# Kernel optimization log

Measured on AMD Instinct MI355X. Metric: run time of the kernel, lower is better.

## Reference

```python
import jax, jax.numpy as jnp
import numpy as np

N_NODES = 50000
N_EDGES = 600000
N_GRAPHS = 500
HID = 128
N_LAYERS = 3
N_CLASSES = 10


def setup_inputs() -> dict:
    key = jax.random.key(0)
    ks = jax.random.split(key, 10)
    x = jax.random.normal(ks[0], (N_NODES, HID), dtype=jnp.float32)
    edge_attr = jax.random.normal(ks[1], (N_EDGES, 4), dtype=jnp.float32)
    edge_index = jax.random.randint(ks[2], (2, N_EDGES), 0, N_NODES, dtype=jnp.int32)
    batch = jnp.sort(jax.random.randint(ks[3], (N_NODES,), 0, N_GRAPHS, dtype=jnp.int32))
    s = 1.0 / np.sqrt(HID)
    Wl = jax.random.normal(ks[4], (N_LAYERS, HID, HID), dtype=jnp.float32) * s
    bl = jax.random.normal(ks[5], (N_LAYERS, HID), dtype=jnp.float32) * s
    Wr = jax.random.normal(ks[6], (N_LAYERS, HID, HID), dtype=jnp.float32) * s
    W1 = jax.random.normal(ks[7], (HID, HID), dtype=jnp.float32) * s
    b1 = jnp.zeros((HID,), dtype=jnp.float32)
    W2 = jax.random.normal(ks[8], (N_CLASSES, HID), dtype=jnp.float32) * s
    b2 = jnp.zeros((N_CLASSES,), dtype=jnp.float32)
    return {"x": x, "edge_attr": edge_attr, "edge_index": edge_index, "batch": batch,
            "Wl": Wl, "bl": bl, "Wr": Wr, "W1": W1, "b1": b1, "W2": W2, "b2": b2}


def _sage_conv(x, src, dst, Wl_i, bl_i, Wr_i):
    # mean aggregation of source-node features at target nodes (PyG SAGEConv)
    msg_sum = jax.ops.segment_sum(x[src], dst, num_segments=N_NODES)  # [N, H]
    cnt = jax.ops.segment_sum(jnp.ones((src.shape[0],), x.dtype), dst, num_segments=N_NODES)
    mean = msg_sum / jnp.maximum(cnt, 1.0)[:, None]
    return mean @ Wl_i.T + bl_i + x @ Wr_i.T


def reference(x, edge_attr, edge_index, batch, Wl, bl, Wr, W1, b1, W2, b2):
    # edge_attr is ignored by SAGEConv
    src, dst = edge_index[0], edge_index[1]
    for i in range(N_LAYERS):
        x = jax.nn.relu(_sage_conv(x, src, dst, Wl[i], bl[i], Wr[i]))
    # global_add_pool over graphs
    g = jax.ops.segment_sum(x, batch, num_segments=N_GRAPHS)  # [G, H]
    g = jax.nn.relu(g)
    # dropout p=0.5 is identity at inference
    h = jax.nn.relu(g @ W1.T + b1)
    logits = h @ W2.T + b2
    return jax.nn.log_softmax(logits, axis=1)
```

## Files before the change

kernel.cpp:

```cpp
#include <hip/hip_runtime.h>
#include <math.h>

#define HID 128
#define NCLS 10
#define MAXDEG 32

typedef __attribute__((ext_vector_type(8))) short frag8;
typedef __attribute__((ext_vector_type(8))) unsigned short u16x8;
typedef __attribute__((ext_vector_type(4))) float f32x4;

static __device__ __forceinline__ float relu_f(float v) { return v > 0.f ? v : 0.f; }

static __device__ __forceinline__ unsigned short f2bf(float f) {
    unsigned int u = __float_as_uint(f);
    u += 0x7fffu + ((u >> 16) & 1u);
    return (unsigned short)(u >> 16);
}
static __device__ __forceinline__ float bf2f(unsigned short u) {
    return __uint_as_float(((unsigned int)u) << 16);
}

static __device__ __forceinline__ void conv4(const float* __restrict__ in,
                                             unsigned short* __restrict__ out, int i) {
    float4 v = *(const float4*)&in[i * 4];
    ushort4 o;
    o.x = f2bf(v.x); o.y = f2bf(v.y); o.z = f2bf(v.z); o.w = f2bf(v.w);
    *(ushort4*)&out[i * 4] = o;
}

__global__ __launch_bounds__(256) void prep_kernel(const float* __restrict__ x, unsigned short* __restrict__ xb, int nx4,
                                                   const float* __restrict__ Wl, unsigned short* __restrict__ wlb, int nwl4,
                                                   const float* __restrict__ Wr, unsigned short* __restrict__ wrb, int nwr4,
                                                   int* __restrict__ deg, int ndeg4) {
    int i = blockIdx.x * blockDim.x + threadIdx.x;
    if (i < nx4) { conv4(x, xb, i); return; }
    i -= nx4;
    if (i < nwl4) { conv4(Wl, wlb, i); return; }
    i -= nwl4;
    if (i < nwr4) { conv4(Wr, wrb, i); return; }
    i -= nwr4;
    if (i < ndeg4) *(int4*)&deg[i * 4] = make_int4(0, 0, 0, 0);
}

__global__ void fill_kernel(const int* __restrict__ src, const int* __restrict__ dst,
                            int* __restrict__ deg, unsigned short* __restrict__ col, int nE) {
    int e = blockIdx.x * blockDim.x + threadIdx.x;
    if (e < nE) {
        int d = dst[e];
        int p = atomicAdd(&deg[d], 1);
        if (p < MAXDEG) col[(long)d * MAXDEG + p] = (unsigned short)src[e];
    }
}

__global__ __launch_bounds__(256) void agg_kernel(const unsigned short* __restrict__ xb,
                                                  const int* __restrict__ deg,
                                                  const unsigned short* __restrict__ col,
                                                  unsigned short* __restrict__ meanb, int nN) {
    int grp = threadIdx.x >> 4;
    int l16 = threadIdx.x & 15;
    int n = blockIdx.x * 16 + grp;
    bool valid = n < nN;
    int d = valid ? min(deg[n], MAXDEG) : 0;
    const unsigned short* cp = col + (long)n * MAXDEG;
    const long fo = (long)l16 * 8;

    float acc[8] = {0, 0, 0, 0, 0, 0, 0, 0};

    int p = 0;
    for (; p + 8 <= d; p += 8) {
        int s0 = cp[p],     s1 = cp[p + 1], s2 = cp[p + 2], s3 = cp[p + 3];
        int s4 = cp[p + 4], s5 = cp[p + 5], s6 = cp[p + 6], s7 = cp[p + 7];
        u16x8 v0 = *(const u16x8*)&xb[(long)s0 * HID + fo];
        u16x8 v1 = *(const u16x8*)&xb[(long)s1 * HID + fo];
        u16x8 v2 = *(const u16x8*)&xb[(long)s2 * HID + fo];
        u16x8 v3 = *(const u16x8*)&xb[(long)s3 * HID + fo];
        u16x8 v4 = *(const u16x8*)&xb[(long)s4 * HID + fo];
        u16x8 v5 = *(const u16x8*)&xb[(long)s5 * HID + fo];
        u16x8 v6 = *(const u16x8*)&xb[(long)s6 * HID + fo];
        u16x8 v7 = *(const u16x8*)&xb[(long)s7 * HID + fo];
#pragma unroll
        for (int j = 0; j < 8; ++j)
            acc[j] += ((bf2f(v0[j]) + bf2f(v1[j])) + (bf2f(v2[j]) + bf2f(v3[j]))) +
                      ((bf2f(v4[j]) + bf2f(v5[j])) + (bf2f(v6[j]) + bf2f(v7[j])));
    }
    if (p + 4 <= d) {
        int s0 = cp[p], s1 = cp[p + 1], s2 = cp[p + 2], s3 = cp[p + 3];
        u16x8 v0 = *(const u16x8*)&xb[(long)s0 * HID + fo];
        u16x8 v1 = *(const u16x8*)&xb[(long)s1 * HID + fo];
        u16x8 v2 = *(const u16x8*)&xb[(long)s2 * HID + fo];
        u16x8 v3 = *(const u16x8*)&xb[(long)s3 * HID + fo];
#pragma unroll
        for (int j = 0; j < 8; ++j)
            acc[j] += (bf2f(v0[j]) + bf2f(v1[j])) + (bf2f(v2[j]) + bf2f(v3[j]));
        p += 4;
    }
    if (p < d) {
        int s0 = cp[p];
        int s1 = cp[min(p + 1, MAXDEG - 1)];
        int s2 = cp[min(p + 2, MAXDEG - 1)];
        int s3 = cp[min(p + 3, MAXDEG - 1)];
        u16x8 v0 = *(const u16x8*)&xb[(long)s0 * HID + fo];
        u16x8 v1 = *(const u16x8*)&xb[(long)s1 * HID + fo];
        u16x8 v2 = *(const u16x8*)&xb[(long)s2 * HID + fo];
        u16x8 v3 = *(const u16x8*)&xb[(long)s3 * HID + fo];
#pragma unroll
        for (int j = 0; j < 8; ++j) acc[j] += bf2f(v0[j]);
        if (p + 1 < d) {
#pragma unroll
            for (int j = 0; j < 8; ++j) acc[j] += bf2f(v1[j]);
        }
        if (p + 2 < d) {
#pragma unroll
            for (int j = 0; j < 8; ++j) acc[j] += bf2f(v2[j]);
        }
        if (p + 3 < d) {
#pragma unroll
            for (int j = 0; j < 8; ++j) acc[j] += bf2f(v3[j]);
        }
    }

    if (valid) {
        float inv = 1.f / fmaxf((float)d, 1.f);
        u16x8 o;
#pragma unroll
        for (int j = 0; j < 8; ++j) o[j] = f2bf(acc[j] * inv);
        *(u16x8*)&meanb[(long)n * HID + fo] = o;
    }
}

__global__ __launch_bounds__(256) void gemm_kernel(const unsigned short* __restrict__ Ab,
                                                   const unsigned short* __restrict__ Xb,
                                                   const unsigned short* __restrict__ Wlb,
                                                   const unsigned short* __restrict__ Wrb,
                                                   const float* __restrict__ bl,
                                                   unsigned short* __restrict__ Yb, int nN) {
    int wave = threadIdx.x >> 6;
    int lane = threadIdx.x & 63;
    int l15 = lane & 15;
    int quad = lane >> 4;
    int r0 = blockIdx.x * 128 + wave * 32;

    f32x4 acc[2][8];
#pragma unroll
    for (int rt = 0; rt < 2; ++rt)
#pragma unroll
        for (int ct = 0; ct < 8; ++ct) acc[rt][ct] = (f32x4){0.f, 0.f, 0.f, 0.f};

#pragma unroll
    for (int ks = 0; ks < HID; ks += 32) {
        frag8 aM[2], aX[2];
#pragma unroll
        for (int rt = 0; rt < 2; ++rt) {
            long row = r0 + rt * 16 + l15;
            aM[rt] = *(const frag8*)&Ab[row * HID + ks + quad * 8];
            aX[rt] = *(const frag8*)&Xb[row * HID + ks + quad * 8];
        }
#pragma unroll
        for (int ct = 0; ct < 8; ++ct) {
            long nrow = ct * 16 + l15;
            frag8 bL = *(const frag8*)&Wlb[nrow * HID + ks + quad * 8];
            frag8 bR = *(const frag8*)&Wrb[nrow * HID + ks + quad * 8];
#pragma unroll
            for (int rt = 0; rt < 2; ++rt) {
                acc[rt][ct] = __builtin_amdgcn_mfma_f32_16x16x32_bf16(aM[rt], bL, acc[rt][ct], 0, 0, 0);
                acc[rt][ct] = __builtin_amdgcn_mfma_f32_16x16x32_bf16(aX[rt], bR, acc[rt][ct], 0, 0, 0);
            }
        }
    }

#pragma unroll
    for (int ct = 0; ct < 8; ++ct) {
        float bb = bl[ct * 16 + l15];
#pragma unroll
        for (int rt = 0; rt < 2; ++rt) {
#pragma unroll
            for (int reg = 0; reg < 4; ++reg) {
                int gm = r0 + rt * 16 + quad * 4 + reg;
                if (gm < nN) {
                    float v = relu_f(acc[rt][ct][reg] + bb);
                    Yb[(long)gm * HID + ct * 16 + l15] = f2bf(v);
                }
            }
        }
    }
}

__global__ __launch_bounds__(128) void poolmlp_kernel(const unsigned short* __restrict__ xb,
                                                      const int* __restrict__ batch, int nN,
                                                      const float* __restrict__ W1,
                                                      const float* __restrict__ b1,
                                                      const float* __restrict__ W2,
                                                      const float* __restrict__ b2,
                                                      float* __restrict__ out) {
    __shared__ float gs[HID];
    __shared__ float hs[HID];
    __shared__ float ls[NCLS];
    __shared__ float red[2];
    int gid = blockIdx.x;
    int j = threadIdx.x;

    int lo = 0, hi = nN;
    while (lo < hi) { int mid = (lo + hi) >> 1; if (batch[mid] < gid) lo = mid + 1; else hi = mid; }
    int s = lo;
    hi = nN;
    while (lo < hi) { int mid = (lo + hi) >> 1; if (batch[mid] < gid + 1) lo = mid + 1; else hi = mid; }
    int e = lo;

    float a0 = 0.f, a1 = 0.f, a2 = 0.f, a3 = 0.f;
    int n = s;
    for (; n + 4 <= e; n += 4) {
        a0 += bf2f(xb[(long)n * HID + j]);
        a1 += bf2f(xb[(long)(n + 1) * HID + j]);
        a2 += bf2f(xb[(long)(n + 2) * HID + j]);
        a3 += bf2f(xb[(long)(n + 3) * HID + j]);
    }
    for (; n < e; ++n) a0 += bf2f(xb[(long)n * HID + j]);
    gs[j] = relu_f((a0 + a1) + (a2 + a3));
    __syncthreads();

    float acc = b1[j];
#pragma unroll 8
    for (int k = 0; k < HID; ++k) acc += gs[k] * W1[j * HID + k];
    hs[j] = relu_f(acc);
    __syncthreads();
    if (j < NCLS) {
        float lg = b2[j];
#pragma unroll 8
        for (int k = 0; k < HID; ++k) lg += hs[k] * W2[j * HID + k];
        ls[j] = lg;
    }
    __syncthreads();
    if (j == 0) {
        float m = ls[0];
        for (int c = 1; c < NCLS; ++c) m = fmaxf(m, ls[c]);
        float sum = 0.f;
        for (int c = 0; c < NCLS; ++c) sum += expf(ls[c] - m);
        red[0] = m;
        red[1] = logf(sum);
    }
    __syncthreads();
    if (j < NCLS) out[gid * NCLS + j] = ls[j] - red[0] - red[1];
}


extern "C" void kernel_launch(void* const* d_in, const int* in_sizes, int n_in,
                              void* d_out, int out_size, void* d_ws, size_t ws_size,
                              hipStream_t stream) {
    const float* x_in  = (const float*)d_in[0];
    const int*   eidx  = (const int*)d_in[2];
    const int*   batch = (const int*)d_in[3];
    const float* Wl    = (const float*)d_in[4];
    const float* bl    = (const float*)d_in[5];
    const float* Wr    = (const float*)d_in[6];
    const float* W1    = (const float*)d_in[7];
    const float* b1    = (const float*)d_in[8];
    const float* W2    = (const float*)d_in[9];
    const float* b2    = (const float*)d_in[10];
    float* out = (float*)d_out;

    const int nN = in_sizes[0] / HID;
    const int nE = in_sizes[2] / 2;
    const int nG = out_size / NCLS;
    const int nWl = in_sizes[4];
    const int nWr = in_sizes[6];
    const int nNp = (nN + 127) & ~127;
    const int nTiles = nNp / 128;

    const int* src = eidx;
    const int* dst = eidx + nE;

    char* p = (char*)d_ws;
    auto carve = [&](size_t bytes) {
        char* r = p;
        p += (bytes + 255) & ~(size_t)255;
        return r;
    };
    unsigned short* xb    = (unsigned short*)carve((size_t)nNp * HID * 2);
    unsigned short* meanb = (unsigned short*)carve((size_t)nNp * HID * 2);
    unsigned short* yb0   = (unsigned short*)carve((size_t)nNp * HID * 2);
    unsigned short* yb1   = (unsigned short*)carve((size_t)nNp * HID * 2);
    unsigned short* wlb   = (unsigned short*)carve((size_t)nWl * 2);
    unsigned short* wrb   = (unsigned short*)carve((size_t)nWr * 2);
    int*   deg    = (int*)carve((size_t)nN * 4);
    unsigned short* col = (unsigned short*)carve((size_t)nN * MAXDEG * 2);
    (void)ws_size; (void)n_in;

    const int nx4 = nN * HID / 4, nwl4 = nWl / 4, nwr4 = nWr / 4, ndeg4 = (nN + 3) / 4;
    const int prep_total = nx4 + nwl4 + nwr4 + ndeg4;
    prep_kernel<<<(prep_total + 255) / 256, 256, 0, stream>>>(
        x_in, xb, nx4, Wl, wlb, nwl4, Wr, wrb, nwr4, deg, ndeg4);

    fill_kernel<<<(nE + 255) / 256, 256, 0, stream>>>(src, dst, deg, col, nE);

    const unsigned short* xcur = xb;
    unsigned short* bufs[2] = {yb0, yb1};
    for (int l = 0; l < 3; ++l) {
        agg_kernel<<<(nN + 15) / 16, 256, 0, stream>>>(xcur, deg, col, meanb, nN);
        gemm_kernel<<<nTiles, 256, 0, stream>>>(
            meanb, xcur, wlb + (size_t)l * HID * HID, wrb + (size_t)l * HID * HID,
            bl + (size_t)l * HID, bufs[l & 1], nN);
        xcur = bufs[l & 1];
    }

    poolmlp_kernel<<<nG, 128, 0, stream>>>(xcur, batch, nN, W1, b1, W2, b2, out);
}
```

Measured before the change: 307.6 us.

## Fuse neighbor mean aggregation into SAGE GEMM via shared-memory tile

Merges the separate aggregation and GEMM kernels into one kernel per layer. Each block gathers the mean features for 64 rows into padded shared memory, syncs, then runs the bf16 MFMA GEMM with four waves split 2x2 over rows and output columns. This drops the global round trip of the mean buffer and one launch per layer. In exchange, tiles are smaller, each block serializes gather latency before its MFMA phase, and the shared-memory tile may limit occupancy.

```diff
diff --git a/kernel.cpp b/kernel.cpp
--- a/kernel.cpp
+++ b/kernel.cpp
@@ -4,6 +4,8 @@
 #define HID 128
 #define NCLS 10
 #define MAXDEG 32
+#define TROWS 64
+#define MSP 136
 
 typedef __attribute__((ext_vector_type(8))) short frag8;
 typedef __attribute__((ext_vector_type(8))) unsigned short u16x8;
@@ -52,112 +54,116 @@
     }
 }
 
-__global__ __launch_bounds__(256) void agg_kernel(const unsigned short* __restrict__ xb,
-                                                  const int* __restrict__ deg,
-                                                  const unsigned short* __restrict__ col,
-                                                  unsigned short* __restrict__ meanb, int nN) {
-    int grp = threadIdx.x >> 4;
-    int l16 = threadIdx.x & 15;
-    int n = blockIdx.x * 16 + grp;
-    bool valid = n < nN;
-    int d = valid ? min(deg[n], MAXDEG) : 0;
-    const unsigned short* cp = col + (long)n * MAXDEG;
-    const long fo = (long)l16 * 8;
-
-    float acc[8] = {0, 0, 0, 0, 0, 0, 0, 0};
-
-    int p = 0;
-    for (; p + 8 <= d; p += 8) {
-        int s0 = cp[p],     s1 = cp[p + 1], s2 = cp[p + 2], s3 = cp[p + 3];
-        int s4 = cp[p + 4], s5 = cp[p + 5], s6 = cp[p + 6], s7 = cp[p + 7];
-        u16x8 v0 = *(const u16x8*)&xb[(long)s0 * HID + fo];
-        u16x8 v1 = *(const u16x8*)&xb[(long)s1 * HID + fo];
-        u16x8 v2 = *(const u16x8*)&xb[(long)s2 * HID + fo];
-        u16x8 v3 = *(const u16x8*)&xb[(long)s3 * HID + fo];
-        u16x8 v4 = *(const u16x8*)&xb[(long)s4 * HID + fo];
-        u16x8 v5 = *(const u16x8*)&xb[(long)s5 * HID + fo];
-        u16x8 v6 = *(const u16x8*)&xb[(long)s6 * HID + fo];
-        u16x8 v7 = *(const u16x8*)&xb[(long)s7 * HID + fo];
-#pragma unroll
-        for (int j = 0; j < 8; ++j)
-            acc[j] += ((bf2f(v0[j]) + bf2f(v1[j])) + (bf2f(v2[j]) + bf2f(v3[j]))) +
-                      ((bf2f(v4[j]) + bf2f(v5[j])) + (bf2f(v6[j]) + bf2f(v7[j])));
-    }
-    if (p + 4 <= d) {
-        int s0 = cp[p], s1 = cp[p + 1], s2 = cp[p + 2], s3 = cp[p + 3];
-        u16x8 v0 = *(const u16x8*)&xb[(long)s0 * HID + fo];
-        u16x8 v1 = *(const u16x8*)&xb[(long)s1 * HID + fo];
-        u16x8 v2 = *(const u16x8*)&xb[(long)s2 * HID + fo];
-        u16x8 v3 = *(const u16x8*)&xb[(long)s3 * HID + fo];
-#pragma unroll
-        for (int j = 0; j < 8; ++j)
-            acc[j] += (bf2f(v0[j]) + bf2f(v1[j])) + (bf2f(v2[j]) + bf2f(v3[j]));
-        p += 4;
-    }
-    if (p < d) {
-        int s0 = cp[p];
-        int s1 = cp[min(p + 1, MAXDEG - 1)];
-        int s2 = cp[min(p + 2, MAXDEG - 1)];
-        int s3 = cp[min(p + 3, MAXDEG - 1)];
-        u16x8 v0 = *(const u16x8*)&xb[(long)s0 * HID + fo];
-        u16x8 v1 = *(const u16x8*)&xb[(long)s1 * HID + fo];
-        u16x8 v2 = *(const u16x8*)&xb[(long)s2 * HID + fo];
-        u16x8 v3 = *(const u16x8*)&xb[(long)s3 * HID + fo];
-#pragma unroll
-        for (int j = 0; j < 8; ++j) acc[j] += bf2f(v0[j]);
-        if (p + 1 < d) {
-#pragma unroll
-            for (int j = 0; j < 8; ++j) acc[j] += bf2f(v1[j]);
+__global__ __launch_bounds__(256, 3) void sage_kernel(const unsigned short* __restrict__ Xb,
+                                                      const int* __restrict__ deg,
+                                                      const unsigned short* __restrict__ col,
+                                                      const unsigned short* __restrict__ Wlb,
+                                                      const unsigned short* __restrict__ Wrb,
+                                                      const float* __restrict__ bl,
+                                                      unsigned short* __restrict__ Yb, int nN) {
+    __shared__ unsigned short ms[TROWS * MSP];
+
+    const int r0 = blockIdx.x * TROWS;
+
+    {
+        const int grp = threadIdx.x >> 4;
+        const int l16 = threadIdx.x & 15;
+        const long fo = (long)l16 * 8;
+        for (int i = 0; i < 4; ++i) {
+            const int nl = grp * 4 + i;
+            const int n = r0 + nl;
+            const int d = (n < nN) ? min(deg[n], MAXDEG) : 0;
+            const unsigned short* cp = col + (long)n * MAXDEG;
+
+            float acc[8] = {0, 0, 0, 0, 0, 0, 0, 0};
+
+            int p = 0;
+            for (; p + 8 <= d; p += 8) {
+                int s0 = cp[p],     s1 = cp[p + 1], s2 = cp[p + 2], s3 = cp[p + 3];
+                int s4 = cp[p + 4], s5 = cp[p + 5], s6 = cp[p + 6], s7 = cp[p + 7];
+                u16x8 v0 = *(const u16x8*)&Xb[(long)s0 * HID + fo];
+                u16x8 v1 = *(const u16x8*)&Xb[(long)s1 * HID + fo];
+                u16x8 v2 = *(const u16x8*)&Xb[(long)s2 * HID + fo];
+                u16x8 v3 = *(const u16x8*)&Xb[(long)s3 * HID + fo];
+                u16x8 v4 = *(const u16x8*)&Xb[(long)s4 * HID + fo];
+                u16x8 v5 = *(const u16x8*)&Xb[(long)s5 * HID + fo];
+                u16x8 v6 = *(const u16x8*)&Xb[(long)s6 * HID + fo];
+                u16x8 v7 = *(const u16x8*)&Xb[(long)s7 * HID + fo];
+#pragma unroll
+                for (int j = 0; j < 8; ++j)
+                    acc[j] += ((bf2f(v0[j]) + bf2f(v1[j])) + (bf2f(v2[j]) + bf2f(v3[j]))) +
+                              ((bf2f(v4[j]) + bf2f(v5[j])) + (bf2f(v6[j]) + bf2f(v7[j])));
+            }
+            if (p + 4 <= d) {
+                int s0 = cp[p], s1 = cp[p + 1], s2 = cp[p + 2], s3 = cp[p + 3];
+                u16x8 v0 = *(const u16x8*)&Xb[(long)s0 * HID + fo];
+                u16x8 v1 = *(const u16x8*)&Xb[(long)s1 * HID + fo];
+                u16x8 v2 = *(const u16x8*)&Xb[(long)s2 * HID + fo];
+                u16x8 v3 = *(const u16x8*)&Xb[(long)s3 * HID + fo];
+#pragma unroll
+                for (int j = 0; j < 8; ++j)
+                    acc[j] += (bf2f(v0[j]) + bf2f(v1[j])) + (bf2f(v2[j]) + bf2f(v3[j]));
+                p += 4;
+            }
+            if (p < d) {
+                int s0 = cp[p];
+                int s1 = cp[min(p + 1, MAXDEG - 1)];
+                int s2 = cp[min(p + 2, MAXDEG - 1)];
+                int s3 = cp[min(p + 3, MAXDEG - 1)];
+                u16x8 v0 = *(const u16x8*)&Xb[(long)s0 * HID + fo];
+                u16x8 v1 = *(const u16x8*)&Xb[(long)s1 * HID + fo];
+                u16x8 v2 = *(const u16x8*)&Xb[(long)s2 * HID + fo];
+                u16x8 v3 = *(const u16x8*)&Xb[(long)s3 * HID + fo];
+#pragma unroll
+                for (int j = 0; j < 8; ++j) acc[j] += bf2f(v0[j]);
+                if (p + 1 < d) {
+#pragma unroll
+                    for (int j = 0; j < 8; ++j) acc[j] += bf2f(v1[j]);
+                }
+                if (p + 2 < d) {
+#pragma unroll
+                    for (int j = 0; j < 8; ++j) acc[j] += bf2f(v2[j]);
+                }
+                if (p + 3 < d) {
+#pragma unroll
+                    for (int j = 0; j < 8; ++j) acc[j] += bf2f(v3[j]);
+                }
+            }
+
+            const float inv = 1.f / fmaxf((float)d, 1.f);
+            u16x8 o;
+#pragma unroll
+            for (int j = 0; j < 8; ++j) o[j] = f2bf(acc[j] * inv);
+            *(u16x8*)&ms[nl * MSP + l16 * 8] = o;
         }
-        if (p + 2 < d) {
-#pragma unroll
-            for (int j = 0; j < 8; ++j) acc[j] += bf2f(v2[j]);
-        }
-        if (p + 3 < d) {
-#pragma unroll
-            for (int j = 0; j < 8; ++j) acc[j] += bf2f(v3[j]);
-        }
-    }
-
-    if (valid) {
-        float inv = 1.f / fmaxf((float)d, 1.f);
-        u16x8 o;
-#pragma unroll
-        for (int j = 0; j < 8; ++j) o[j] = f2bf(acc[j] * inv);
-        *(u16x8*)&meanb[(long)n * HID + fo] = o;
-    }
-}
-
-__global__ __launch_bounds__(256) void gemm_kernel(const unsigned short* __restrict__ Ab,
-                                                   const unsigned short* __restrict__ Xb,
-                                                   const unsigned short* __restrict__ Wlb,
-                                                   const unsigned short* __restrict__ Wrb,
-                                                   const float* __restrict__ bl,
-                                                   unsigned short* __restrict__ Yb, int nN) {
-    int wave = threadIdx.x >> 6;
-    int lane = threadIdx.x & 63;
-    int l15 = lane & 15;
-    int quad = lane >> 4;
-    int r0 = blockIdx.x * 128 + wave * 32;
-
-    f32x4 acc[2][8];
+    }
+    __syncthreads();
+
+    const int lane = threadIdx.x & 63;
+    const int wave = threadIdx.x >> 6;
+    const int l15 = lane & 15;
+    const int quad = lane >> 4;
+    const int wr = wave & 1;
+    const int wc = wave >> 1;
+
+    f32x4 acc[2][4];
 #pragma unroll
     for (int rt = 0; rt < 2; ++rt)
 #pragma unroll
-        for (int ct = 0; ct < 8; ++ct) acc[rt][ct] = (f32x4){0.f, 0.f, 0.f, 0.f};
+        for (int ct = 0; ct < 4; ++ct) acc[rt][ct] = (f32x4){0.f, 0.f, 0.f, 0.f};
 
 #pragma unroll
     for (int ks = 0; ks < HID; ks += 32) {
         frag8 aM[2], aX[2];
 #pragma unroll
         for (int rt = 0; rt < 2; ++rt) {
-            long row = r0 + rt * 16 + l15;
-            aM[rt] = *(const frag8*)&Ab[row * HID + ks + quad * 8];
-            aX[rt] = *(const frag8*)&Xb[row * HID + ks + quad * 8];
+            const int lrow = wr * 32 + rt * 16 + l15;
+            aM[rt] = *(const frag8*)&ms[lrow * MSP + ks + quad * 8];
+            aX[rt] = *(const frag8*)&Xb[(long)(r0 + lrow) * HID + ks + quad * 8];
         }
 #pragma unroll
-        for (int ct = 0; ct < 8; ++ct) {
-            long nrow = ct * 16 + l15;
+        for (int ct = 0; ct < 4; ++ct) {
+            const long nrow = wc * 64 + ct * 16 + l15;
             frag8 bL = *(const frag8*)&Wlb[nrow * HID + ks + quad * 8];
             frag8 bR = *(const frag8*)&Wrb[nrow * HID + ks + quad * 8];
 #pragma unroll
@@ -169,16 +175,17 @@
     }
 
 #pragma unroll
-    for (int ct = 0; ct < 8; ++ct) {
-        float bb = bl[ct * 16 + l15];
+    for (int ct = 0; ct < 4; ++ct) {
+        const int gc = wc * 64 + ct * 16 + l15;
+        const float bb = bl[gc];
 #pragma unroll
         for (int rt = 0; rt < 2; ++rt) {
 #pragma unroll
             for (int reg = 0; reg < 4; ++reg) {
-                int gm = r0 + rt * 16 + quad * 4 + reg;
+                const int gm = r0 + wr * 32 + rt * 16 + quad * 4 + reg;
                 if (gm < nN) {
-                    float v = relu_f(acc[rt][ct][reg] + bb);
-                    Yb[(long)gm * HID + ct * 16 + l15] = f2bf(v);
+                    const float v = relu_f(acc[rt][ct][reg] + bb);
+                    Yb[(long)gm * HID + gc] = f2bf(v);
                 }
             }
         }
@@ -263,8 +270,8 @@
     const int nG = out_size / NCLS;
     const int nWl = in_sizes[4];
     const int nWr = in_sizes[6];
-    const int nNp = (nN + 127) & ~127;
-    const int nTiles = nNp / 128;
+    const int nNp = (nN + TROWS - 1) & ~(TROWS - 1);
+    const int nTiles = nNp / TROWS;
 
     const int* src = eidx;
     const int* dst = eidx + nE;
@@ -275,13 +282,12 @@
         p += (bytes + 255) & ~(size_t)255;
         return r;
     };
-    unsigned short* xb    = (unsigned short*)carve((size_t)nNp * HID * 2);
-    unsigned short* meanb = (unsigned short*)carve((size_t)nNp * HID * 2);
-    unsigned short* yb0   = (unsigned short*)carve((size_t)nNp * HID * 2);
-    unsigned short* yb1   = (unsigned short*)carve((size_t)nNp * HID * 2);
-    unsigned short* wlb   = (unsigned short*)carve((size_t)nWl * 2);
-    unsigned short* wrb   = (unsigned short*)carve((size_t)nWr * 2);
-    int*   deg    = (int*)carve((size_t)nN * 4);
+    unsigned short* xb  = (unsigned short*)carve((size_t)nNp * HID * 2);
+    unsigned short* yb0 = (unsigned short*)carve((size_t)nNp * HID * 2);
+    unsigned short* yb1 = (unsigned short*)carve((size_t)nNp * HID * 2);
+    unsigned short* wlb = (unsigned short*)carve((size_t)nWl * 2);
+    unsigned short* wrb = (unsigned short*)carve((size_t)nWr * 2);
+    int*   deg = (int*)carve((size_t)nN * 4);
     unsigned short* col = (unsigned short*)carve((size_t)nN * MAXDEG * 2);
     (void)ws_size; (void)n_in;
 
@@ -295,9 +301,9 @@
     const unsigned short* xcur = xb;
     unsigned short* bufs[2] = {yb0, yb1};
     for (int l = 0; l < 3; ++l) {
-        agg_kernel<<<(nN + 15) / 16, 256, 0, stream>>>(xcur, deg, col, meanb, nN);
-        gemm_kernel<<<nTiles, 256, 0, stream>>>(
-            meanb, xcur, wlb + (size_t)l * HID * HID, wrb + (size_t)l * HID * HID,
+        sage_kernel<<<nTiles, 256, 0, stream>>>(
+            xcur, deg, col,
+            wlb + (size_t)l * HID * HID, wrb + (size_t)l * HID * HID,
             bl + (size_t)l * HID, bufs[l & 1], nN);
         xcur = bufs[l & 1];
     }
```

After: 284.4 us. 7.5% less time.
